# Optimization experiments

Hardware: AMD Instinct MI355X
Metric: run time of the kernel (lower is better)

The kernel has to match this reference:

```python
import jax, jax.numpy as jnp
from jax import lax
import numpy as np

NEG_SLOPE = 0.01  # PyTorch LeakyReLU default


def setup_inputs() -> dict:
    key = jax.random.key(0)
    ks = jax.random.split(key, 7)
    B, Ns, T, C = 32, 512, 128, 25
    proj_dim, H = 20, 25
    s_lin = 1.0 / np.sqrt(C)
    s_gru = 1.0 / np.sqrt(H)
    return {
        "x": jax.random.normal(ks[0], (B, Ns, T, C), jnp.float32),
        "W1": jax.random.uniform(ks[1], (proj_dim, C), jnp.float32, -s_lin, s_lin),
        "b1": jax.random.uniform(ks[2], (proj_dim,), jnp.float32, -s_lin, s_lin),
        "W_ih": jax.random.uniform(ks[3], (3 * H, proj_dim), jnp.float32, -s_gru, s_gru),
        "W_hh": jax.random.uniform(ks[4], (3 * H, H), jnp.float32, -s_gru, s_gru),
        "b_ih": jax.random.uniform(ks[5], (3 * H,), jnp.float32, -s_gru, s_gru),
        "b_hh": jax.random.uniform(ks[6], (3 * H,), jnp.float32, -s_gru, s_gru),
    }


def reference(x, W1, b1, W_ih, W_hh, b_ih, b_hh):
    # Linear + LeakyReLU projection: [B, Ns, T, 25] -> [B, Ns, T, proj_dim]
    p = jnp.einsum("bntc,pc->bntp", x, W1) + b1
    p = jnp.where(p >= 0, p, NEG_SLOPE * p)

    B, Ns, T, P = p.shape
    H = W_hh.shape[1]
    p = p.reshape(B * Ns, T, P)

    # Precompute input-side gate pre-activations for all timesteps: [N, T, 3H]
    gx = jnp.einsum("ntp,gp->ntg", p, W_ih) + b_ih
    gx = jnp.swapaxes(gx, 0, 1)  # [T, N, 3H] for scan

    def step(h, gx_t):
        gh = h @ W_hh.T + b_hh  # [N, 3H]
        xr, xz, xn = jnp.split(gx_t, 3, axis=-1)
        hr, hz, hn = jnp.split(gh, 3, axis=-1)
        r = jax.nn.sigmoid(xr + hr)
        z = jax.nn.sigmoid(xz + hz)
        n = jnp.tanh(xn + r * hn)
        h_new = (1.0 - z) * n + z * h
        return h_new, None

    h0 = jnp.zeros((B * Ns, H), p.dtype)
    hT, _ = lax.scan(step, h0, gx)
    return hT.reshape(B, Ns, H)
```

## Files before the change

### kernel.cpp

```cpp
#include <hip/hip_runtime.h>


typedef __bf16 bf16x8 __attribute__((ext_vector_type(8)));
typedef float  f32x4  __attribute__((ext_vector_type(4)));

#define TT 128
#define CC 25
#define PP 20
#define HH 25
#define NSEQ 16384
#define S  36
#define MFMA __builtin_amdgcn_mfma_f32_16x16x32_bf16

__device__ __forceinline__ void split2(float f, __bf16& hi, __bf16& lo) {
    hi = (__bf16)f;
    lo = (__bf16)(f - (float)hi);
}
__device__ __forceinline__ float sigm(float v) { return 1.f / (1.f + __expf(-v)); }

__global__ __launch_bounds__(128, 2) void gru_pc(
    const float* __restrict__ x,   const float* __restrict__ W1,
    const float* __restrict__ b1,  const float* __restrict__ Wih,
    const float* __restrict__ Whh, const float* __restrict__ bih,
    const float* __restrict__ bhh, float* __restrict__ out)
{
    __shared__ float sp[16 * S];
    __shared__ float sh[2][16 * S];
    __shared__ f32x4 sgx[2][3][2][4][16];

    const int tid  = threadIdx.x;
    const int wid  = tid >> 6;
    const bool pw  = (wid == 0);
    const int lane = tid & 63;
    const int m = lane & 15, q = lane >> 4;
    const int n0 = blockIdx.x * 16;

    for (int idx = tid; idx < 16 * S; idx += 128) {
        sp[idx] = 0.f; sh[0][idx] = 0.f; sh[1][idx] = 0.f;
    }
    __syncthreads();
    if (tid < 16) {
        sp[tid * S + PP]    = 1.0f;
        sh[0][tid * S + HH] = 1.0f;
        sh[1][tid * S + HH] = 1.0f;
    }
    __syncthreads();

    bf16x8 WgH[6], WgL[6], WpH[2], WpL[2];
    {
        const float* Ws = pw ? Wih : Whh;
        const float* bs = pw ? bih : bhh;
        const int kd    = pw ? PP  : HH;
        #pragma unroll
        for (int tt = 0; tt < 6; ++tt) {
            const int g = tt >> 1;
            const int u = (tt & 1) * 16 + m;
            const bool uv = (u < HH);
            const int row = g * HH + u;
            bf16x8 h8, l8;
            #pragma unroll
            for (int j = 0; j < 8; ++j) {
                const int k = q * 8 + j;
                float v = 0.f;
                if (uv) {
                    if (k < kd)       v = Ws[row * kd + k];
                    else if (k == kd) v = bs[row];
                }
                __bf16 a, b; split2(v, a, b); h8[j] = a; l8[j] = b;
            }
            WgH[tt] = h8; WgL[tt] = l8;
        }
    }
    if (pw) {
        #pragma unroll
        for (int tt = 0; tt < 2; ++tt) {
            const int u = tt * 16 + m;
            const bool uv = (u < PP);
            bf16x8 h8, l8;
            #pragma unroll
            for (int j = 0; j < 8; ++j) {
                const int k = q * 8 + j;
                float v = 0.f;
                if (uv) {
                    if (k < CC)       v = W1[u * CC + k];
                    else if (k == CC) v = b1[u];
                }
                __bf16 a, b; split2(v, a, b); h8[j] = a; l8[j] = b;
            }
            WpH[tt] = h8; WpL[tt] = l8;
        }
    }

    const float* xrow = x + (size_t)(n0 + m) * (TT * CC);
    float xc[8];

    auto produce = [&](int tc) {
        bf16x8 xH, xL;
        #pragma unroll
        for (int j = 0; j < 8; ++j) { __bf16 a,b; split2(xc[j],a,b); xH[j]=a; xL[j]=b; }

        {
            const int tn = (tc + 1 < TT) ? tc + 1 : TT - 1;
            const float* xr = xrow + tn * CC;
            #pragma unroll
            for (int j = 0; j < 8; ++j) {
                const int k = q * 8 + j;
                if (k < CC) xc[j] = xr[k];
            }
        }

        f32x4 p0 = {0.f,0.f,0.f,0.f}, p1 = {0.f,0.f,0.f,0.f};
        p0 = MFMA(WpH[0], xH, p0, 0,0,0);
        p0 = MFMA(WpH[0], xL, p0, 0,0,0);
        p0 = MFMA(WpL[0], xH, p0, 0,0,0);
        p1 = MFMA(WpH[1], xH, p1, 0,0,0);
        p1 = MFMA(WpH[1], xL, p1, 0,0,0);
        p1 = MFMA(WpL[1], xH, p1, 0,0,0);
        #pragma unroll
        for (int r = 0; r < 4; ++r) {
            p0[r] = (p0[r] >= 0.f) ? p0[r] : 0.01f * p0[r];
            p1[r] = (p1[r] >= 0.f) ? p1[r] : 0.01f * p1[r];
        }

        *(f32x4*)(sp + m * S + 4 * q) = p0;
        if (q == 0) *(f32x4*)(sp + m * S + 16) = p1;

        f32x4 pa = ((const f32x4*)(sp + m * S + 8 * q))[0];
        f32x4 pb = ((const f32x4*)(sp + m * S + 8 * q))[1];
        bf16x8 pH, pL;
        #pragma unroll
        for (int j = 0; j < 4; ++j) {
            __bf16 a, b;
            split2(pa[j], a, b); pH[j]   = a; pL[j]   = b;
            split2(pb[j], a, b); pH[4+j] = a; pL[4+j] = b;
        }

        const int s = tc & 1;
        #pragma unroll
        for (int tp = 0; tp < 2; ++tp) {
            f32x4 acc = {0.f,0.f,0.f,0.f};
            acc = MFMA(WgH[tp], pH, acc, 0,0,0);
            acc = MFMA(WgH[tp], pL, acc, 0,0,0);
            acc = MFMA(WgL[tp], pH, acc, 0,0,0);
            sgx[s][0][tp][q][m] = acc;
            f32x4 az = {0.f,0.f,0.f,0.f};
            az = MFMA(WgH[2+tp], pH, az, 0,0,0);
            az = MFMA(WgH[2+tp], pL, az, 0,0,0);
            az = MFMA(WgL[2+tp], pH, az, 0,0,0);
            sgx[s][1][tp][q][m] = az;
            f32x4 an = {0.f,0.f,0.f,0.f};
            an = MFMA(WgH[4+tp], pH, an, 0,0,0);
            an = MFMA(WgH[4+tp], pL, an, 0,0,0);
            an = MFMA(WgL[4+tp], pH, an, 0,0,0);
            sgx[s][2][tp][q][m] = an;
        }
    };

    float ho[2][4] = {{0.f,0.f,0.f,0.f},{0.f,0.f,0.f,0.f}};

    auto consume = [&](int t) {
        const float* hrow = sh[t & 1] + m * S + 8 * q;
        f32x4 ha = ((const f32x4*)hrow)[0];
        f32x4 hb = ((const f32x4*)hrow)[1];
        bf16x8 hH, hL;
        #pragma unroll
        for (int j = 0; j < 4; ++j) {
            __bf16 a, b;
            split2(ha[j], a, b); hH[j]   = a; hL[j]   = b;
            split2(hb[j], a, b); hH[4+j] = a; hL[4+j] = b;
        }
        const int s = t & 1;
        f32x4 aR[2], aZ[2], aHn[2], gN[2];
        #pragma unroll
        for (int tp = 0; tp < 2; ++tp) {
            f32x4 acc = sgx[s][0][tp][q][m];
            acc = MFMA(WgH[tp], hH, acc, 0,0,0);
            acc = MFMA(WgH[tp], hL, acc, 0,0,0);
            acc = MFMA(WgL[tp], hH, acc, 0,0,0);
            aR[tp] = acc;
            f32x4 az = sgx[s][1][tp][q][m];
            az = MFMA(WgH[2+tp], hH, az, 0,0,0);
            az = MFMA(WgH[2+tp], hL, az, 0,0,0);
            az = MFMA(WgL[2+tp], hH, az, 0,0,0);
            aZ[tp] = az;
            gN[tp] = sgx[s][2][tp][q][m];
            f32x4 ah = {0.f,0.f,0.f,0.f};
            ah = MFMA(WgH[4+tp], hH, ah, 0,0,0);
            ah = MFMA(WgH[4+tp], hL, ah, 0,0,0);
            ah = MFMA(WgL[4+tp], hH, ah, 0,0,0);
            aHn[tp] = ah;
        }
        #pragma unroll
        for (int tp = 0; tp < 2; ++tp) {
            f32x4 hv;
            #pragma unroll
            for (int r = 0; r < 4; ++r) {
                const float rg = sigm(aR[tp][r]);
                const float zg = sigm(aZ[tp][r]);
                const float nv = gN[tp][r] + rg * aHn[tp][r];
                const float e  = __expf(-2.f * nv);
                const float ng = 2.f / (1.f + e) - 1.f;
                const float h2 = zg * (ho[tp][r] - ng) + ng;
                ho[tp][r] = h2; hv[r] = h2;
            }
            float* dst = sh[(t + 1) & 1] + m * S + tp * 16 + 4 * q;
            if (tp == 0) {
                *(f32x4*)dst = hv;
            } else {
                if (q < 2)       *(f32x4*)dst = hv;
                else if (q == 2) dst[0] = hv[0];
            }
        }
    };

    if (pw) {
        #pragma unroll
        for (int j = 0; j < 8; ++j) {
            const int k = q * 8 + j;
            xc[j] = (k < CC) ? xrow[k] : (k == CC ? 1.0f : 0.f);
        }
        produce(0);
    }
    __syncthreads();

    for (int t = 0; t < TT; ++t) {
        if (pw) {
            if (t + 1 < TT) produce(t + 1);
        } else {
            consume(t);
        }
        __syncthreads();
    }

    if (!pw) {
        float* orow = out + (size_t)(n0 + m) * HH;
        #pragma unroll
        for (int tp = 0; tp < 2; ++tp) {
            #pragma unroll
            for (int r = 0; r < 4; ++r) {
                const int u = tp * 16 + 4 * q + r;
                if (u < HH) orow[u] = ho[tp][r];
            }
        }
    }
}

extern "C" void kernel_launch(void* const* d_in, const int* in_sizes, int n_in,
                              void* d_out, int out_size, void* d_ws, size_t ws_size,
                              hipStream_t stream) {
    const float* x   = (const float*)d_in[0];
    const float* W1  = (const float*)d_in[1];
    const float* b1  = (const float*)d_in[2];
    const float* Wih = (const float*)d_in[3];
    const float* Whh = (const float*)d_in[4];
    const float* bih = (const float*)d_in[5];
    const float* bhh = (const float*)d_in[6];
    float* out = (float*)d_out;

    gru_pc<<<NSEQ / 16, 128, 0, stream>>>(x, W1, b1, Wih, Whh, bih, bhh, out);
}
```

Before: 421.7 us.

## Replace per-step block barriers with LDS flag ring between producer and consumer waves

After: 395.2 us. 6.3% less time.

```diff
diff --git a/kernel.cpp b/kernel.cpp
--- a/kernel.cpp
+++ b/kernel.cpp
@@ -11,6 +11,8 @@
 #define NSEQ 16384
 #define S  36
 #define MFMA __builtin_amdgcn_mfma_f32_16x16x32_bf16
+#define LD_ACQ(p)    __hip_atomic_load((p), __ATOMIC_ACQUIRE, __HIP_MEMORY_SCOPE_WORKGROUP)
+#define ST_REL(p, v) __hip_atomic_store((p), (v), __ATOMIC_RELEASE, __HIP_MEMORY_SCOPE_WORKGROUP)
 
 __device__ __forceinline__ void split2(float f, __bf16& hi, __bf16& lo) {
     hi = (__bf16)f;
@@ -18,7 +20,7 @@
 }
 __device__ __forceinline__ float sigm(float v) { return 1.f / (1.f + __expf(-v)); }
 
-__global__ __launch_bounds__(128, 2) void gru_pc(
+__global__ __launch_bounds__(128, 2) void gru_ring(
     const float* __restrict__ x,   const float* __restrict__ W1,
     const float* __restrict__ b1,  const float* __restrict__ Wih,
     const float* __restrict__ Whh, const float* __restrict__ bih,
@@ -26,11 +28,11 @@
 {
     __shared__ float sp[16 * S];
     __shared__ float sh[2][16 * S];
-    __shared__ f32x4 sgx[2][3][2][4][16];
+    __shared__ f32x4 sgx[4][3][2][4][16];
+    __shared__ int s_prod, s_cons;
 
     const int tid  = threadIdx.x;
-    const int wid  = tid >> 6;
-    const bool pw  = (wid == 0);
+    const bool pw  = (tid < 64);
     const int lane = tid & 63;
     const int m = lane & 15, q = lane >> 4;
     const int n0 = blockIdx.x * 16;
@@ -38,6 +40,7 @@
     for (int idx = tid; idx < 16 * S; idx += 128) {
         sp[idx] = 0.f; sh[0][idx] = 0.f; sh[1][idx] = 0.f;
     }
+    if (tid == 0) { s_prod = 0; s_cons = 0; }
     __syncthreads();
     if (tid < 16) {
         sp[tid * S + PP]    = 1.0f;
@@ -91,148 +94,154 @@
         }
     }
 
-    const float* xrow = x + (size_t)(n0 + m) * (TT * CC);
-    float xc[8];
-
-    auto produce = [&](int tc) {
-        bf16x8 xH, xL;
-        #pragma unroll
-        for (int j = 0; j < 8; ++j) { __bf16 a,b; split2(xc[j],a,b); xH[j]=a; xL[j]=b; }
-
-        {
-            const int tn = (tc + 1 < TT) ? tc + 1 : TT - 1;
-            const float* xr = xrow + tn * CC;
+    if (pw) {
+        const float* xrow = x + (size_t)(n0 + m) * (TT * CC);
+        const int cbase = (q < 3) ? q * 8 : 21;
+        float xc[8];
+
+        auto load_x = [&](int t) {
+            const float* xr = xrow + t * CC;
+            f32x4 va = *(const f32x4*)(xr + cbase);
+            f32x4 vb = *(const f32x4*)(xr + cbase + ((q < 3) ? 4 : 0));
             #pragma unroll
             for (int j = 0; j < 8; ++j) {
-                const int k = q * 8 + j;
-                if (k < CC) xc[j] = xr[k];
-            }
-        }
-
-        f32x4 p0 = {0.f,0.f,0.f,0.f}, p1 = {0.f,0.f,0.f,0.f};
-        p0 = MFMA(WpH[0], xH, p0, 0,0,0);
-        p0 = MFMA(WpH[0], xL, p0, 0,0,0);
-        p0 = MFMA(WpL[0], xH, p0, 0,0,0);
-        p1 = MFMA(WpH[1], xH, p1, 0,0,0);
-        p1 = MFMA(WpH[1], xL, p1, 0,0,0);
-        p1 = MFMA(WpL[1], xH, p1, 0,0,0);
-        #pragma unroll
-        for (int r = 0; r < 4; ++r) {
-            p0[r] = (p0[r] >= 0.f) ? p0[r] : 0.01f * p0[r];
-            p1[r] = (p1[r] >= 0.f) ? p1[r] : 0.01f * p1[r];
-        }
-
-        *(f32x4*)(sp + m * S + 4 * q) = p0;
-        if (q == 0) *(f32x4*)(sp + m * S + 16) = p1;
-
-        f32x4 pa = ((const f32x4*)(sp + m * S + 8 * q))[0];
-        f32x4 pb = ((const f32x4*)(sp + m * S + 8 * q))[1];
-        bf16x8 pH, pL;
-        #pragma unroll
-        for (int j = 0; j < 4; ++j) {
-            __bf16 a, b;
-            split2(pa[j], a, b); pH[j]   = a; pL[j]   = b;
-            split2(pb[j], a, b); pH[4+j] = a; pL[4+j] = b;
-        }
-
-        const int s = tc & 1;
-        #pragma unroll
-        for (int tp = 0; tp < 2; ++tp) {
-            f32x4 acc = {0.f,0.f,0.f,0.f};
-            acc = MFMA(WgH[tp], pH, acc, 0,0,0);
-            acc = MFMA(WgH[tp], pL, acc, 0,0,0);
-            acc = MFMA(WgL[tp], pH, acc, 0,0,0);
-            sgx[s][0][tp][q][m] = acc;
-            f32x4 az = {0.f,0.f,0.f,0.f};
-            az = MFMA(WgH[2+tp], pH, az, 0,0,0);
-            az = MFMA(WgH[2+tp], pL, az, 0,0,0);
-            az = MFMA(WgL[2+tp], pH, az, 0,0,0);
-            sgx[s][1][tp][q][m] = az;
-            f32x4 an = {0.f,0.f,0.f,0.f};
-            an = MFMA(WgH[4+tp], pH, an, 0,0,0);
-            an = MFMA(WgH[4+tp], pL, an, 0,0,0);
-            an = MFMA(WgL[4+tp], pH, an, 0,0,0);
-            sgx[s][2][tp][q][m] = an;
-        }
-    };
-
-    float ho[2][4] = {{0.f,0.f,0.f,0.f},{0.f,0.f,0.f,0.f}};
-
-    auto consume = [&](int t) {
-        const float* hrow = sh[t & 1] + m * S + 8 * q;
-        f32x4 ha = ((const f32x4*)hrow)[0];
-        f32x4 hb = ((const f32x4*)hrow)[1];
-        bf16x8 hH, hL;
-        #pragma unroll
-        for (int j = 0; j < 4; ++j) {
-            __bf16 a, b;
-            split2(ha[j], a, b); hH[j]   = a; hL[j]   = b;
-            split2(hb[j], a, b); hH[4+j] = a; hL[4+j] = b;
-        }
-        const int s = t & 1;
-        f32x4 aR[2], aZ[2], aHn[2], gN[2];
-        #pragma unroll
-        for (int tp = 0; tp < 2; ++tp) {
-            f32x4 acc = sgx[s][0][tp][q][m];
-            acc = MFMA(WgH[tp], hH, acc, 0,0,0);
-            acc = MFMA(WgH[tp], hL, acc, 0,0,0);
-            acc = MFMA(WgL[tp], hH, acc, 0,0,0);
-            aR[tp] = acc;
-            f32x4 az = sgx[s][1][tp][q][m];
-            az = MFMA(WgH[2+tp], hH, az, 0,0,0);
-            az = MFMA(WgH[2+tp], hL, az, 0,0,0);
-            az = MFMA(WgL[2+tp], hH, az, 0,0,0);
-            aZ[tp] = az;
-            gN[tp] = sgx[s][2][tp][q][m];
-            f32x4 ah = {0.f,0.f,0.f,0.f};
-            ah = MFMA(WgH[4+tp], hH, ah, 0,0,0);
-            ah = MFMA(WgH[4+tp], hL, ah, 0,0,0);
-            ah = MFMA(WgL[4+tp], hH, ah, 0,0,0);
-            aHn[tp] = ah;
-        }
-        #pragma unroll
-        for (int tp = 0; tp < 2; ++tp) {
-            f32x4 hv;
+                float v;
+                if (q < 3) v = (j < 4) ? va[j] : vb[j - 4];
+                else       v = (j == 0) ? va[3] : (j == 1 ? 1.0f : 0.0f);
+                xc[j] = v;
+            }
+        };
+
+        auto produce = [&](int tc) {
+            bf16x8 xH, xL;
+            #pragma unroll
+            for (int j = 0; j < 8; ++j) { __bf16 a,b; split2(xc[j],a,b); xH[j]=a; xL[j]=b; }
+
+            {
+                const int tn = (tc + 1 < TT) ? tc + 1 : TT - 1;
+                load_x(tn);
+            }
+
+            f32x4 p0 = {0.f,0.f,0.f,0.f}, p1 = {0.f,0.f,0.f,0.f};
+            p0 = MFMA(WpH[0], xH, p0, 0,0,0);
+            p0 = MFMA(WpH[0], xL, p0, 0,0,0);
+            p0 = MFMA(WpL[0], xH, p0, 0,0,0);
+            p1 = MFMA(WpH[1], xH, p1, 0,0,0);
+            p1 = MFMA(WpH[1], xL, p1, 0,0,0);
+            p1 = MFMA(WpL[1], xH, p1, 0,0,0);
             #pragma unroll
             for (int r = 0; r < 4; ++r) {
-                const float rg = sigm(aR[tp][r]);
-                const float zg = sigm(aZ[tp][r]);
-                const float nv = gN[tp][r] + rg * aHn[tp][r];
-                const float e  = __expf(-2.f * nv);
-                const float ng = 2.f / (1.f + e) - 1.f;
-                const float h2 = zg * (ho[tp][r] - ng) + ng;
-                ho[tp][r] = h2; hv[r] = h2;
-            }
-            float* dst = sh[(t + 1) & 1] + m * S + tp * 16 + 4 * q;
-            if (tp == 0) {
-                *(f32x4*)dst = hv;
-            } else {
-                if (q < 2)       *(f32x4*)dst = hv;
-                else if (q == 2) dst[0] = hv[0];
-            }
-        }
-    };
-
-    if (pw) {
-        #pragma unroll
-        for (int j = 0; j < 8; ++j) {
-            const int k = q * 8 + j;
-            xc[j] = (k < CC) ? xrow[k] : (k == CC ? 1.0f : 0.f);
-        }
-        produce(0);
-    }
-    __syncthreads();
-
-    for (int t = 0; t < TT; ++t) {
-        if (pw) {
-            if (t + 1 < TT) produce(t + 1);
-        } else {
-            consume(t);
-        }
-        __syncthreads();
-    }
-
-    if (!pw) {
+                p0[r] = (p0[r] >= 0.f) ? p0[r] : 0.01f * p0[r];
+                p1[r] = (p1[r] >= 0.f) ? p1[r] : 0.01f * p1[r];
+            }
+
+            *(f32x4*)(sp + m * S + 4 * q) = p0;
+            if (q == 0) *(f32x4*)(sp + m * S + 16) = p1;
+
+            f32x4 pa = ((const f32x4*)(sp + m * S + 8 * q))[0];
+            f32x4 pb = ((const f32x4*)(sp + m * S + 8 * q))[1];
+            bf16x8 pH, pL;
+            #pragma unroll
+            for (int j = 0; j < 4; ++j) {
+                __bf16 a, b;
+                split2(pa[j], a, b); pH[j]   = a; pL[j]   = b;
+                split2(pb[j], a, b); pH[4+j] = a; pL[4+j] = b;
+            }
+
+            const int s = tc & 3;
+            #pragma unroll
+            for (int tp = 0; tp < 2; ++tp) {
+                f32x4 acc = {0.f,0.f,0.f,0.f};
+                acc = MFMA(WgH[tp], pH, acc, 0,0,0);
+                acc = MFMA(WgH[tp], pL, acc, 0,0,0);
+                acc = MFMA(WgL[tp], pH, acc, 0,0,0);
+                sgx[s][0][tp][q][m] = acc;
+                f32x4 az = {0.f,0.f,0.f,0.f};
+                az = MFMA(WgH[2+tp], pH, az, 0,0,0);
+                az = MFMA(WgH[2+tp], pL, az, 0,0,0);
+                az = MFMA(WgL[2+tp], pH, az, 0,0,0);
+                sgx[s][1][tp][q][m] = az;
+                f32x4 an = {0.f,0.f,0.f,0.f};
+                an = MFMA(WgH[4+tp], pH, an, 0,0,0);
+                an = MFMA(WgH[4+tp], pL, an, 0,0,0);
+                an = MFMA(WgL[4+tp], pH, an, 0,0,0);
+                sgx[s][2][tp][q][m] = an;
+            }
+        };
+
+        load_x(0);
+        int known_cons = 0;
+        for (int t = 0; t < TT; ++t) {
+            if (t >= 4 && known_cons < t - 3) {
+                do { known_cons = LD_ACQ(&s_cons); } while (known_cons < t - 3);
+            }
+            produce(t);
+            if (lane == 0) ST_REL(&s_prod, t + 1);
+        }
+    } else {
+        float ho[2][4] = {{0.f,0.f,0.f,0.f},{0.f,0.f,0.f,0.f}};
+        int known_prod = 0;
+
+        for (int t = 0; t < TT; ++t) {
+            if (known_prod < t + 1) {
+                do { known_prod = LD_ACQ(&s_prod); } while (known_prod < t + 1);
+            }
+
+            const float* hrow = sh[t & 1] + m * S + 8 * q;
+            f32x4 ha = ((const f32x4*)hrow)[0];
+            f32x4 hb = ((const f32x4*)hrow)[1];
+            bf16x8 hH, hL;
+            #pragma unroll
+            for (int j = 0; j < 4; ++j) {
+                __bf16 a, b;
+                split2(ha[j], a, b); hH[j]   = a; hL[j]   = b;
+                split2(hb[j], a, b); hH[4+j] = a; hL[4+j] = b;
+            }
+            const int s = t & 3;
+            f32x4 aR[2], aZ[2], aHn[2], gN[2];
+            #pragma unroll
+            for (int tp = 0; tp < 2; ++tp) {
+                f32x4 acc = sgx[s][0][tp][q][m];
+                acc = MFMA(WgH[tp], hH, acc, 0,0,0);
+                acc = MFMA(WgH[tp], hL, acc, 0,0,0);
+                acc = MFMA(WgL[tp], hH, acc, 0,0,0);
+                aR[tp] = acc;
+                f32x4 az = sgx[s][1][tp][q][m];
+                az = MFMA(WgH[2+tp], hH, az, 0,0,0);
+                az = MFMA(WgH[2+tp], hL, az, 0,0,0);
+                az = MFMA(WgL[2+tp], hH, az, 0,0,0);
+                aZ[tp] = az;
+                gN[tp] = sgx[s][2][tp][q][m];
+                f32x4 ah = {0.f,0.f,0.f,0.f};
+                ah = MFMA(WgH[4+tp], hH, ah, 0,0,0);
+                ah = MFMA(WgH[4+tp], hL, ah, 0,0,0);
+                ah = MFMA(WgL[4+tp], hH, ah, 0,0,0);
+                aHn[tp] = ah;
+            }
+            #pragma unroll
+            for (int tp = 0; tp < 2; ++tp) {
+                f32x4 hv;
+                #pragma unroll
+                for (int r = 0; r < 4; ++r) {
+                    const float rg = sigm(aR[tp][r]);
+                    const float zg = sigm(aZ[tp][r]);
+                    const float nv = gN[tp][r] + rg * aHn[tp][r];
+                    const float e  = __expf(-2.f * nv);
+                    const float ng = 2.f / (1.f + e) - 1.f;
+                    const float h2 = zg * (ho[tp][r] - ng) + ng;
+                    ho[tp][r] = h2; hv[r] = h2;
+                }
+                float* dst = sh[(t + 1) & 1] + m * S + tp * 16 + 4 * q;
+                if (tp == 0) {
+                    *(f32x4*)dst = hv;
+                } else {
+                    if (q < 2)       *(f32x4*)dst = hv;
+                    else if (q == 2) dst[0] = hv[0];
+                }
+            }
+            if (lane == 0) ST_REL(&s_cons, t + 1);
+        }
+
         float* orow = out + (size_t)(n0 + m) * HH;
         #pragma unroll
         for (int tp = 0; tp < 2; ++tp) {
@@ -257,5 +266,5 @@
     const float* bhh = (const float*)d_in[6];
     float* out = (float*)d_out;
 
-    gru_pc<<<NSEQ / 16, 128, 0, stream>>>(x, W1, b1, Wih, Whh, bih, bhh, out);
+    gru_ring<<<NSEQ / 16, 128, 0, stream>>>(x, W1, b1, Wih, Whh, bih, bhh, out);
 }
```
